# Performance work log

Hardware: AMD Instinct MI355X
Metric: run time of the kernel (lower is better)

Reference implementation:

```python
import jax, jax.numpy as jnp
import numpy as np

BITS = 8
EPS = 1e-5


def round_clip(x, lo, hi):
    # round-then-clip with straight-through estimator (matches Audyn's round_clip)
    return x + jax.lax.stop_gradient(jnp.clip(jnp.round(x), lo, hi) - x)


def setup_inputs() -> dict:
    key = jax.random.key(0)
    kx, kw = jax.random.split(key)
    B, S, D_IN, D_OUT = 4, 2048, 4096, 16384
    x = jax.random.normal(kx, (B, S, D_IN), dtype=jnp.float32)
    # kaiming-uniform-ish scale: bound = 1/sqrt(in_features)
    bound = 1.0 / np.sqrt(D_IN)
    weight = jax.random.uniform(kw, (D_OUT, D_IN), dtype=jnp.float32,
                                minval=-bound, maxval=bound)
    return {"x": x, "weight": weight}


def reference(x, weight):
    q = float(2 ** (BITS - 1))  # 128
    # activation quantization: per-tensor abs-max
    gamma = jnp.maximum(jnp.max(jnp.abs(x)), EPS)
    xq = round_clip(x * (q / gamma), -q, q - 1.0)
    # weight quantization: per-tensor mean-abs (NB: source divides abs_weight, not weight)
    abs_w = jnp.abs(weight)
    beta = jnp.maximum(jnp.mean(abs_w), EPS)
    wq = round_clip(abs_w / beta, -1.0, 1.0)
    # GEMM (no bias: source always registers bias as None) + rescale
    y = jnp.einsum("bsd,od->bso", xq, wq)
    return y * (beta * gamma / q)
```

## Files before the change

### kernel.cpp

```cpp
#include <hip/hip_runtime.h>

typedef float f32x4 __attribute__((ext_vector_type(4)));
typedef int   i32x4 __attribute__((ext_vector_type(4)));
typedef char  s8x16 __attribute__((ext_vector_type(16)));

#define GAS __attribute__((address_space(1)))
#define LAS __attribute__((address_space(3)))

constexpr int M = 8192;
constexpr int N = 16384;
constexpr int K = 4096;
constexpr long long NX = (long long)M * K;
constexpr long long NW = (long long)N * K;
constexpr int NPART = 2048;


__global__ void reduce_absmax_kernel(const float* __restrict__ x,
                                     unsigned* __restrict__ gmax, int n4) {
  float m = 0.f;
  int stride = gridDim.x * blockDim.x;
  for (int i = blockIdx.x * blockDim.x + threadIdx.x; i < n4; i += stride) {
    f32x4 v = *(const f32x4*)(x + (size_t)i * 4);
    m = fmaxf(m, fmaxf(fmaxf(fabsf(v[0]), fabsf(v[1])),
                       fmaxf(fabsf(v[2]), fabsf(v[3]))));
  }
#pragma unroll
  for (int off = 32; off > 0; off >>= 1) m = fmaxf(m, __shfl_down(m, off));
  __shared__ float sm[4];
  int lane = threadIdx.x & 63, wid = threadIdx.x >> 6;
  if (lane == 0) sm[wid] = m;
  __syncthreads();
  if (threadIdx.x == 0) {
    m = fmaxf(fmaxf(sm[0], sm[1]), fmaxf(sm[2], sm[3]));
    atomicMax(gmax, __float_as_uint(m));
  }
}

__global__ void reduce_abssum_kernel(const float* __restrict__ w,
                                     float* __restrict__ partials, int n4) {
  float s = 0.f;
  int stride = gridDim.x * blockDim.x;
  for (int i = blockIdx.x * blockDim.x + threadIdx.x; i < n4; i += stride) {
    f32x4 v = *(const f32x4*)(w + (size_t)i * 4);
    s += fabsf(v[0]) + fabsf(v[1]) + fabsf(v[2]) + fabsf(v[3]);
  }
#pragma unroll
  for (int off = 32; off > 0; off >>= 1) s += __shfl_down(s, off);
  __shared__ float sm[4];
  int lane = threadIdx.x & 63, wid = threadIdx.x >> 6;
  if (lane == 0) sm[wid] = s;
  __syncthreads();
  if (threadIdx.x == 0) partials[blockIdx.x] = (sm[0] + sm[1]) + (sm[2] + sm[3]);
}

__global__ void finalize_kernel(const unsigned* __restrict__ gbits,
                                const float* __restrict__ partials,
                                float* __restrict__ params) {
  __shared__ double sd[256];
  double s = 0.0;
  for (int i = threadIdx.x; i < NPART; i += 256) s += (double)partials[i];
  sd[threadIdx.x] = s;
  __syncthreads();
  for (int h = 128; h > 0; h >>= 1) {
    if (threadIdx.x < h) sd[threadIdx.x] += sd[threadIdx.x + h];
    __syncthreads();
  }
  if (threadIdx.x == 0) {
    float beta  = fmaxf((float)(sd[0] / (double)NW), 1e-5f);
    float gamma = fmaxf(__uint_as_float(gbits[0]), 1e-5f);
    params[0] = 128.0f / gamma;
    params[1] = beta;
    params[2] = beta * gamma / 128.0f;
  }
}


__global__ void quant_x_kernel(const float* __restrict__ x,
                               char* __restrict__ xq,
                               const float* __restrict__ params, int n16) {
  float s = params[0];
  int stride = gridDim.x * blockDim.x;
  for (int i = blockIdx.x * blockDim.x + threadIdx.x; i < n16; i += stride) {
    const f32x4* p = (const f32x4*)(x + (size_t)i * 16);
    s8x16 o;
#pragma unroll
    for (int v = 0; v < 4; ++v) {
      f32x4 t = p[v];
#pragma unroll
      for (int k = 0; k < 4; ++k) {
        float r = fminf(fmaxf(rintf(t[k] * s), -128.f), 127.f);
        o[v * 4 + k] = (char)(int)r;
      }
    }
    *(s8x16*)(xq + (size_t)i * 16) = o;
  }
}

__global__ void quant_w_kernel(const float* __restrict__ w,
                               char* __restrict__ wq,
                               const float* __restrict__ params, int n16) {
  float beta = params[1];
  int stride = gridDim.x * blockDim.x;
  for (int i = blockIdx.x * blockDim.x + threadIdx.x; i < n16; i += stride) {
    const f32x4* p = (const f32x4*)(w + (size_t)i * 16);
    s8x16 o;
#pragma unroll
    for (int v = 0; v < 4; ++v) {
      f32x4 t = p[v];
#pragma unroll
      for (int k = 0; k < 4; ++k) {
        o[v * 4 + k] = (rintf(fabsf(t[k]) / beta) >= 1.0f) ? (char)1 : (char)0;
      }
    }
    *(s8x16*)(wq + (size_t)i * 16) = o;
  }
}


__global__ __launch_bounds__(512, 2) void gemm_kernel(
    const char* __restrict__ A,
    const char* __restrict__ B,
    float* __restrict__ C,
    const float* __restrict__ params) {
  __shared__ __align__(16) char lds[131072];

  const int tid  = threadIdx.x;
  const int lane = tid & 63, wid = tid >> 6;
  const int wm = wid >> 2, wn = wid & 3;
  const int r16 = lane & 15, q4 = lane >> 4;

  const int wg = (blockIdx.x & 7) * 256 + (blockIdx.x >> 3);
  const int m0 = (wg >> 6) * 256, n0 = (wg & 63) * 256;

  const int l8 = lane >> 3;
  const int cswz = ((lane & 7) ^ l8) * 16;
  const char* Ar = A + (size_t)(m0 + wid * 16 + l8) * K + cswz;
  const char* Br = B + (size_t)(n0 + wid * 16 + l8) * K + cswz;
  const int dbase = wid * 2048 + lane * 16;

  auto stage = [&](int t, int b) {
    char* L = lds + b * 65536;
    const char* a0 = Ar + t * 128;
    const char* b0 = Br + t * 128;
    __builtin_amdgcn_global_load_lds((const GAS void*)(a0),               (LAS void*)(L + dbase),                16, 0, 0);
    __builtin_amdgcn_global_load_lds((const GAS void*)(a0 + 8 * K),       (LAS void*)(L + dbase + 1024),         16, 0, 0);
    __builtin_amdgcn_global_load_lds((const GAS void*)(a0 + 128 * K),     (LAS void*)(L + dbase + 16384),        16, 0, 0);
    __builtin_amdgcn_global_load_lds((const GAS void*)(a0 + 136 * K),     (LAS void*)(L + dbase + 17408),        16, 0, 0);
    __builtin_amdgcn_global_load_lds((const GAS void*)(b0),               (LAS void*)(L + dbase + 32768),        16, 0, 0);
    __builtin_amdgcn_global_load_lds((const GAS void*)(b0 + 8 * K),       (LAS void*)(L + dbase + 33792),        16, 0, 0);
    __builtin_amdgcn_global_load_lds((const GAS void*)(b0 + 128 * K),     (LAS void*)(L + dbase + 49152),        16, 0, 0);
    __builtin_amdgcn_global_load_lds((const GAS void*)(b0 + 136 * K),     (LAS void*)(L + dbase + 50176),        16, 0, 0);
  };

  int aoff[8][2], boff[4][2];
#pragma unroll
  for (int i = 0; i < 8; ++i)
#pragma unroll
    for (int kh = 0; kh < 2; ++kh)
      aoff[i][kh] = (wm * 128 + i * 16 + r16) * 128 + (((kh * 4 + q4) ^ (r16 & 7)) * 16);
#pragma unroll
  for (int j = 0; j < 4; ++j)
#pragma unroll
    for (int kh = 0; kh < 2; ++kh)
      boff[j][kh] = 32768 + (wn * 64 + j * 16 + r16) * 128 + (((kh * 4 + q4) ^ (r16 & 7)) * 16);

  i32x4 acc[8][4] = {};
  i32x4 afr[8], bfr0, bfr1;

  stage(0, 0);

  for (int t = 0; t < 32; ++t) {
    const char* buf = lds + (t & 1) * 65536;
    asm volatile("s_waitcnt vmcnt(0)" ::: "memory");
    __builtin_amdgcn_sched_barrier(0);
    __builtin_amdgcn_s_barrier();
    __builtin_amdgcn_sched_barrier(0);
    if (t + 1 < 32) stage(t + 1, (t + 1) & 1);
#pragma unroll
    for (int i = 0; i < 8; ++i) afr[i] = *(const i32x4*)(buf + aoff[i][0]);
    bfr0 = *(const i32x4*)(buf + boff[0][0]);
    bfr1 = *(const i32x4*)(buf + boff[1][0]);
    __builtin_amdgcn_s_setprio(1);
#pragma unroll
    for (int i = 0; i < 8; ++i) {
      acc[i][0] = __builtin_amdgcn_mfma_i32_16x16x64_i8(afr[i], bfr0, acc[i][0], 0, 0, 0);
      acc[i][1] = __builtin_amdgcn_mfma_i32_16x16x64_i8(afr[i], bfr1, acc[i][1], 0, 0, 0);
    }
    __builtin_amdgcn_s_setprio(0);
    __builtin_amdgcn_s_barrier();
    bfr0 = *(const i32x4*)(buf + boff[2][0]);
    bfr1 = *(const i32x4*)(buf + boff[3][0]);
    __builtin_amdgcn_s_setprio(1);
#pragma unroll
    for (int i = 0; i < 8; ++i) {
      acc[i][2] = __builtin_amdgcn_mfma_i32_16x16x64_i8(afr[i], bfr0, acc[i][2], 0, 0, 0);
      acc[i][3] = __builtin_amdgcn_mfma_i32_16x16x64_i8(afr[i], bfr1, acc[i][3], 0, 0, 0);
    }
    __builtin_amdgcn_s_setprio(0);
    __builtin_amdgcn_s_barrier();
#pragma unroll
    for (int i = 0; i < 8; ++i) afr[i] = *(const i32x4*)(buf + aoff[i][1]);
    bfr0 = *(const i32x4*)(buf + boff[0][1]);
    bfr1 = *(const i32x4*)(buf + boff[1][1]);
    __builtin_amdgcn_s_setprio(1);
#pragma unroll
    for (int i = 0; i < 8; ++i) {
      acc[i][0] = __builtin_amdgcn_mfma_i32_16x16x64_i8(afr[i], bfr0, acc[i][0], 0, 0, 0);
      acc[i][1] = __builtin_amdgcn_mfma_i32_16x16x64_i8(afr[i], bfr1, acc[i][1], 0, 0, 0);
    }
    __builtin_amdgcn_s_setprio(0);
    __builtin_amdgcn_s_barrier();
    bfr0 = *(const i32x4*)(buf + boff[2][1]);
    bfr1 = *(const i32x4*)(buf + boff[3][1]);
    __builtin_amdgcn_s_setprio(1);
#pragma unroll
    for (int i = 0; i < 8; ++i) {
      acc[i][2] = __builtin_amdgcn_mfma_i32_16x16x64_i8(afr[i], bfr0, acc[i][2], 0, 0, 0);
      acc[i][3] = __builtin_amdgcn_mfma_i32_16x16x64_i8(afr[i], bfr1, acc[i][3], 0, 0, 0);
    }
    __builtin_amdgcn_s_setprio(0);
  }

  const float sc = params[2];
  const int crow = m0 + wm * 128 + q4 * 4;
  const int ccol = n0 + wn * 64 + r16;
#pragma unroll
  for (int i = 0; i < 8; ++i)
#pragma unroll
    for (int jj = 0; jj < 4; ++jj)
#pragma unroll
      for (int r = 0; r < 4; ++r)
        C[(size_t)(crow + i * 16 + r) * N + (ccol + jj * 16)] = (float)acc[i][jj][r] * sc;
}


extern "C" void kernel_launch(void* const* d_in, const int* in_sizes, int n_in,
                              void* d_out, int out_size, void* d_ws, size_t ws_size,
                              hipStream_t stream) {
  const float* x = (const float*)d_in[0];
  const float* w = (const float*)d_in[1];
  float* out = (float*)d_out;
  char* ws = (char*)d_ws;

  unsigned* gamma_bits = (unsigned*)ws;
  float*    params     = (float*)(ws + 16);
  float*    partials   = (float*)(ws + 256);
  char*     xq = ws + 16384;
  char*     wq = ws + 16384 + (size_t)NX;

  hipMemsetAsync(ws, 0, 256, stream);

  reduce_absmax_kernel<<<NPART, 256, 0, stream>>>(x, gamma_bits, (int)(NX / 4));
  reduce_abssum_kernel<<<NPART, 256, 0, stream>>>(w, partials, (int)(NW / 4));
  finalize_kernel<<<1, 256, 0, stream>>>(gamma_bits, partials, params);
  quant_x_kernel<<<2048, 256, 0, stream>>>(x, xq, params, (int)(NX / 16));
  quant_w_kernel<<<2048, 256, 0, stream>>>(w, wq, params, (int)(NW / 16));

  gemm_kernel<<<2048, 512, 0, stream>>>(xq, wq, out, params);
}
```

Measured before the change: 765.2 us.

## Stagger int8 GEMM tile loads across four MFMA phases with deeper prefetch

The GEMM main loop is restructured so each k-tile's global-to-LDS loads are split into four quarter-chunks. Each chunk is issued during a different MFMA phase, and the first chunk of tile t+2 is prefetched into the buffer just freed. Fragment reads are regrouped into 4x2 sub-blocks with explicit lgkmcnt waits and barriers around each phase. The intent is to spread VMEM issue evenly and replace the single vmcnt(0) stall per tile with a partial wait. The cost is more barriers per iteration and a tighter hand-written schedule; the launch bounds also drop the min-2-blocks hint.

```diff
diff --git a/kernel.cpp b/kernel.cpp
--- a/kernel.cpp
+++ b/kernel.cpp
@@ -13,6 +13,7 @@
 constexpr long long NX = (long long)M * K;
 constexpr long long NW = (long long)N * K;
 constexpr int NPART = 2048;
+constexpr int NKT = 32;
 
 
 __global__ void reduce_absmax_kernel(const float* __restrict__ x,
@@ -117,7 +118,9 @@
 }
 
 
-__global__ __launch_bounds__(512, 2) void gemm_kernel(
+#define SBAR __builtin_amdgcn_sched_barrier(0)
+
+__global__ __launch_bounds__(512) void gemm_kernel(
     const char* __restrict__ A,
     const char* __restrict__ B,
     float* __restrict__ C,
@@ -132,93 +135,110 @@
   const int wg = (blockIdx.x & 7) * 256 + (blockIdx.x >> 3);
   const int m0 = (wg >> 6) * 256, n0 = (wg & 63) * 256;
 
-  const int l8 = lane >> 3;
-  const int cswz = ((lane & 7) ^ l8) * 16;
-  const char* Ar = A + (size_t)(m0 + wid * 16 + l8) * K + cswz;
-  const char* Br = B + (size_t)(n0 + wid * 16 + l8) * K + cswz;
-  const int dbase = wid * 2048 + lane * 16;
-
-  auto stage = [&](int t, int b) {
-    char* L = lds + b * 65536;
-    const char* a0 = Ar + t * 128;
-    const char* b0 = Br + t * 128;
-    __builtin_amdgcn_global_load_lds((const GAS void*)(a0),               (LAS void*)(L + dbase),                16, 0, 0);
-    __builtin_amdgcn_global_load_lds((const GAS void*)(a0 + 8 * K),       (LAS void*)(L + dbase + 1024),         16, 0, 0);
-    __builtin_amdgcn_global_load_lds((const GAS void*)(a0 + 128 * K),     (LAS void*)(L + dbase + 16384),        16, 0, 0);
-    __builtin_amdgcn_global_load_lds((const GAS void*)(a0 + 136 * K),     (LAS void*)(L + dbase + 17408),        16, 0, 0);
-    __builtin_amdgcn_global_load_lds((const GAS void*)(b0),               (LAS void*)(L + dbase + 32768),        16, 0, 0);
-    __builtin_amdgcn_global_load_lds((const GAS void*)(b0 + 8 * K),       (LAS void*)(L + dbase + 33792),        16, 0, 0);
-    __builtin_amdgcn_global_load_lds((const GAS void*)(b0 + 128 * K),     (LAS void*)(L + dbase + 49152),        16, 0, 0);
-    __builtin_amdgcn_global_load_lds((const GAS void*)(b0 + 136 * K),     (LAS void*)(L + dbase + 50176),        16, 0, 0);
+  const int csw = ((lane & 7) ^ ((lane >> 3) & 7)) * 16;
+  const char* gA = A + (size_t)(m0 + wid * 32 + (lane >> 3)) * K + csw;
+  const char* gB = B + (size_t)(n0 + wid * 32 + (lane >> 3)) * K + csw;
+  const int dA = wid * 4096 + lane * 16;
+  const int dB = 32768 + dA;
+
+  auto stg = [&](int t, int q) {
+    char* L = lds + (t & 1) * 65536;
+    const size_t go = (size_t)q * 8 * K + (size_t)t * 128;
+    __builtin_amdgcn_global_load_lds((const GAS void*)(gA + go), (LAS void*)(L + dA + q * 1024), 16, 0, 0);
+    __builtin_amdgcn_global_load_lds((const GAS void*)(gB + go), (LAS void*)(L + dB + q * 1024), 16, 0, 0);
   };
 
-  int aoff[8][2], boff[4][2];
-#pragma unroll
-  for (int i = 0; i < 8; ++i)
-#pragma unroll
-    for (int kh = 0; kh < 2; ++kh)
-      aoff[i][kh] = (wm * 128 + i * 16 + r16) * 128 + (((kh * 4 + q4) ^ (r16 & 7)) * 16);
-#pragma unroll
-  for (int j = 0; j < 4; ++j)
-#pragma unroll
-    for (int kh = 0; kh < 2; ++kh)
-      boff[j][kh] = 32768 + (wn * 64 + j * 16 + r16) * 128 + (((kh * 4 + q4) ^ (r16 & 7)) * 16);
+  const int abase = (wm * 128 + r16) * 128;
+  const int bbase = 32768 + (wn * 64 + r16) * 128;
+  const int sw0 = ((q4) ^ (r16 & 7)) * 16;
+  const int sw1 = ((4 + q4) ^ (r16 & 7)) * 16;
 
   i32x4 acc[8][4] = {};
-  i32x4 afr[8], bfr0, bfr1;
-
-  stage(0, 0);
-
-  for (int t = 0; t < 32; ++t) {
+  i32x4 af[4][2], bf[4][2];
+
+  stg(0, 0); stg(0, 1); stg(0, 2); stg(0, 3);
+  stg(1, 0);
+  asm volatile("s_waitcnt vmcnt(2)" ::: "memory");
+  SBAR; __builtin_amdgcn_s_barrier(); SBAR;
+
+  for (int t = 0; t < NKT; ++t) {
     const char* buf = lds + (t & 1) * 65536;
-    asm volatile("s_waitcnt vmcnt(0)" ::: "memory");
-    __builtin_amdgcn_sched_barrier(0);
-    __builtin_amdgcn_s_barrier();
-    __builtin_amdgcn_sched_barrier(0);
-    if (t + 1 < 32) stage(t + 1, (t + 1) & 1);
-#pragma unroll
-    for (int i = 0; i < 8; ++i) afr[i] = *(const i32x4*)(buf + aoff[i][0]);
-    bfr0 = *(const i32x4*)(buf + boff[0][0]);
-    bfr1 = *(const i32x4*)(buf + boff[1][0]);
-    __builtin_amdgcn_s_setprio(1);
-#pragma unroll
-    for (int i = 0; i < 8; ++i) {
-      acc[i][0] = __builtin_amdgcn_mfma_i32_16x16x64_i8(afr[i], bfr0, acc[i][0], 0, 0, 0);
-      acc[i][1] = __builtin_amdgcn_mfma_i32_16x16x64_i8(afr[i], bfr1, acc[i][1], 0, 0, 0);
-    }
-    __builtin_amdgcn_s_setprio(0);
-    __builtin_amdgcn_s_barrier();
-    bfr0 = *(const i32x4*)(buf + boff[2][0]);
-    bfr1 = *(const i32x4*)(buf + boff[3][0]);
-    __builtin_amdgcn_s_setprio(1);
-#pragma unroll
-    for (int i = 0; i < 8; ++i) {
-      acc[i][2] = __builtin_amdgcn_mfma_i32_16x16x64_i8(afr[i], bfr0, acc[i][2], 0, 0, 0);
-      acc[i][3] = __builtin_amdgcn_mfma_i32_16x16x64_i8(afr[i], bfr1, acc[i][3], 0, 0, 0);
-    }
-    __builtin_amdgcn_s_setprio(0);
-    __builtin_amdgcn_s_barrier();
-#pragma unroll
-    for (int i = 0; i < 8; ++i) afr[i] = *(const i32x4*)(buf + aoff[i][1]);
-    bfr0 = *(const i32x4*)(buf + boff[0][1]);
-    bfr1 = *(const i32x4*)(buf + boff[1][1]);
-    __builtin_amdgcn_s_setprio(1);
-#pragma unroll
-    for (int i = 0; i < 8; ++i) {
-      acc[i][0] = __builtin_amdgcn_mfma_i32_16x16x64_i8(afr[i], bfr0, acc[i][0], 0, 0, 0);
-      acc[i][1] = __builtin_amdgcn_mfma_i32_16x16x64_i8(afr[i], bfr1, acc[i][1], 0, 0, 0);
-    }
-    __builtin_amdgcn_s_setprio(0);
-    __builtin_amdgcn_s_barrier();
-    bfr0 = *(const i32x4*)(buf + boff[2][1]);
-    bfr1 = *(const i32x4*)(buf + boff[3][1]);
-    __builtin_amdgcn_s_setprio(1);
-#pragma unroll
-    for (int i = 0; i < 8; ++i) {
-      acc[i][2] = __builtin_amdgcn_mfma_i32_16x16x64_i8(afr[i], bfr0, acc[i][2], 0, 0, 0);
-      acc[i][3] = __builtin_amdgcn_mfma_i32_16x16x64_i8(afr[i], bfr1, acc[i][3], 0, 0, 0);
-    }
-    __builtin_amdgcn_s_setprio(0);
+#pragma unroll
+    for (int i = 0; i < 4; ++i) {
+      af[i][0] = *(const i32x4*)(buf + abase + i * 2048 + sw0);
+      af[i][1] = *(const i32x4*)(buf + abase + i * 2048 + sw1);
+    }
+#pragma unroll
+    for (int j = 0; j < 2; ++j) {
+      bf[j][0] = *(const i32x4*)(buf + bbase + j * 2048 + sw0);
+      bf[j][1] = *(const i32x4*)(buf + bbase + j * 2048 + sw1);
+    }
+    if (t + 1 < NKT) stg(t + 1, 1);
+    SBAR; __builtin_amdgcn_s_barrier(); SBAR;
+    asm volatile("s_waitcnt lgkmcnt(0)" ::: "memory"); SBAR;
+    __builtin_amdgcn_s_setprio(1);
+#pragma unroll
+    for (int kh = 0; kh < 2; ++kh)
+#pragma unroll
+      for (int i = 0; i < 4; ++i)
+#pragma unroll
+        for (int j = 0; j < 2; ++j)
+          acc[i][j] = __builtin_amdgcn_mfma_i32_16x16x64_i8(af[i][kh], bf[j][kh], acc[i][j], 0, 0, 0);
+    __builtin_amdgcn_s_setprio(0);
+    SBAR; __builtin_amdgcn_s_barrier(); SBAR;
+#pragma unroll
+    for (int j = 2; j < 4; ++j) {
+      bf[j][0] = *(const i32x4*)(buf + bbase + j * 2048 + sw0);
+      bf[j][1] = *(const i32x4*)(buf + bbase + j * 2048 + sw1);
+    }
+    if (t + 1 < NKT) stg(t + 1, 2);
+    SBAR; __builtin_amdgcn_s_barrier(); SBAR;
+    asm volatile("s_waitcnt lgkmcnt(0)" ::: "memory"); SBAR;
+    __builtin_amdgcn_s_setprio(1);
+#pragma unroll
+    for (int kh = 0; kh < 2; ++kh)
+#pragma unroll
+      for (int i = 0; i < 4; ++i)
+#pragma unroll
+        for (int j = 2; j < 4; ++j)
+          acc[i][j] = __builtin_amdgcn_mfma_i32_16x16x64_i8(af[i][kh], bf[j][kh], acc[i][j], 0, 0, 0);
+    __builtin_amdgcn_s_setprio(0);
+    SBAR; __builtin_amdgcn_s_barrier(); SBAR;
+#pragma unroll
+    for (int i = 0; i < 4; ++i) {
+      af[i][0] = *(const i32x4*)(buf + abase + (i + 4) * 2048 + sw0);
+      af[i][1] = *(const i32x4*)(buf + abase + (i + 4) * 2048 + sw1);
+    }
+    if (t + 1 < NKT) stg(t + 1, 3);
+    SBAR; __builtin_amdgcn_s_barrier(); SBAR;
+    asm volatile("s_waitcnt lgkmcnt(0)" ::: "memory"); SBAR;
+    __builtin_amdgcn_s_setprio(1);
+#pragma unroll
+    for (int kh = 0; kh < 2; ++kh)
+#pragma unroll
+      for (int i = 0; i < 4; ++i)
+#pragma unroll
+        for (int j = 0; j < 2; ++j)
+          acc[i + 4][j] = __builtin_amdgcn_mfma_i32_16x16x64_i8(af[i][kh], bf[j][kh], acc[i + 4][j], 0, 0, 0);
+    __builtin_amdgcn_s_setprio(0);
+    SBAR; __builtin_amdgcn_s_barrier(); SBAR;
+    if (t + 2 < NKT) stg(t + 2, 0);
+    if (t < NKT - 2) {
+      asm volatile("s_waitcnt vmcnt(2)" ::: "memory");
+    } else {
+      asm volatile("s_waitcnt vmcnt(0)" ::: "memory");
+    }
+    SBAR; __builtin_amdgcn_s_barrier(); SBAR;
+    __builtin_amdgcn_s_setprio(1);
+#pragma unroll
+    for (int kh = 0; kh < 2; ++kh)
+#pragma unroll
+      for (int i = 0; i < 4; ++i)
+#pragma unroll
+        for (int j = 2; j < 4; ++j)
+          acc[i + 4][j] = __builtin_amdgcn_mfma_i32_16x16x64_i8(af[i][kh], bf[j][kh], acc[i + 4][j], 0, 0, 0);
+    __builtin_amdgcn_s_setprio(0);
+    SBAR; __builtin_amdgcn_s_barrier(); SBAR;
   }
 
   const float sc = params[2];
@@ -227,10 +247,10 @@
 #pragma unroll
   for (int i = 0; i < 8; ++i)
 #pragma unroll
-    for (int jj = 0; jj < 4; ++jj)
+    for (int j = 0; j < 4; ++j)
 #pragma unroll
       for (int r = 0; r < 4; ++r)
-        C[(size_t)(crow + i * 16 + r) * N + (ccol + jj * 16)] = (float)acc[i][jj][r] * sc;
+        C[(size_t)(crow + i * 16 + r) * N + (ccol + j * 16)] = (float)acc[i][j][r] * sc;
 }
 
 
```

Measured after the change: 757.5 us. No clear change (-1.0%).
